# Performance work log

Hardware: AMD Instinct MI355X
Metric: run time of the kernel (lower is better)

## Reference

```python
import jax, jax.numpy as jnp
import numpy as np

OUT_SIZE = 7          # output_size
RATIO = 2             # sampling_ratio
STRIDES = (4, 8, 16, 32)  # feature_map_strides, levels P2..P5
CANONICAL = 224.0


def _bilinear_sample(fm, ys, xs):
    """fm: [H,W,C]; ys: [R,K]; xs: [R,K] -> [R,K,K,C] samples at (y[r,ky], x[r,kx]).
    Out-of-range points (y<=-1 or y>=H, same for x) produce 0, matching ROIAlign."""
    H, W, C = fm.shape
    vy = (ys > -1.0) & (ys < H)
    vx = (xs > -1.0) & (xs < W)
    y = jnp.clip(ys, 0.0, H - 1.0)
    x = jnp.clip(xs, 0.0, W - 1.0)
    y0 = jnp.floor(y).astype(jnp.int32)
    x0 = jnp.floor(x).astype(jnp.int32)
    y1 = jnp.minimum(y0 + 1, H - 1)
    x1 = jnp.minimum(x0 + 1, W - 1)
    ly = y - y0; hy = 1.0 - ly  # [R,K]
    lx = x - x0; hx = 1.0 - lx
    f00 = fm[y0[:, :, None], x0[:, None, :]]  # [R,Ky,Kx,C]
    f01 = fm[y0[:, :, None], x1[:, None, :]]
    f10 = fm[y1[:, :, None], x0[:, None, :]]
    f11 = fm[y1[:, :, None], x1[:, None, :]]
    w00 = (hy[:, :, None] * hx[:, None, :])[..., None]
    w01 = (hy[:, :, None] * lx[:, None, :])[..., None]
    w10 = (ly[:, :, None] * hx[:, None, :])[..., None]
    w11 = (ly[:, :, None] * lx[:, None, :])[..., None]
    val = w00 * f00 + w01 * f01 + w10 * f10 + w11 * f11
    mask = (vy[:, :, None] & vx[:, None, :])[..., None]
    return jnp.where(mask, val, 0.0)


def _roi_align_one(fm, boxes):
    """fm: [H,W,C]; boxes: [R,4] in this feature map's coords -> [R,C,S,S]."""
    x1, y1, x2, y2 = boxes[:, 0], boxes[:, 1], boxes[:, 2], boxes[:, 3]
    rw = jnp.maximum(x2 - x1, 1.0)
    rh = jnp.maximum(y2 - y1, 1.0)
    S, r = OUT_SIZE, RATIO
    K = S * r
    g = (jnp.arange(K, dtype=jnp.float32) + 0.5) / r  # sample grid in bin units
    ys = y1[:, None] + g[None, :] * (rh / S)[:, None]  # [R,K]
    xs = x1[:, None] + g[None, :] * (rw / S)[:, None]
    v = _bilinear_sample(fm, ys, xs)                   # [R,K,K,C]
    R_ = v.shape[0]; C = fm.shape[-1]
    v = v.reshape(R_, S, r, S, r, C).mean(axis=(2, 4))  # avg over sampling points
    return v.transpose(0, 3, 1, 2)                      # [R,C,S,S]


def setup_inputs() -> dict:
    key = jax.random.key(0)
    ks = jax.random.split(key, 5)
    B, C, N = 4, 256, 512
    fm2 = jax.random.normal(ks[0], (B, 256, 256, C), dtype=jnp.float32)
    fm3 = jax.random.normal(ks[1], (B, 128, 128, C), dtype=jnp.float32)
    fm4 = jax.random.normal(ks[2], (B, 64, 64, C), dtype=jnp.float32)
    fm5 = jax.random.normal(ks[3], (B, 32, 32, C), dtype=jnp.float32)
    pts = jax.random.uniform(ks[4], (B, N, 2, 2), minval=0.0, maxval=1024.0)
    lo = jnp.min(pts, axis=2)  # [B,N,2] -> (x1,y1)
    hi = jnp.max(pts, axis=2)  # [B,N,2] -> (x2,y2)
    rois = jnp.concatenate([lo, hi], axis=-1)  # [B,N,4]
    return {"fm2": fm2, "fm3": fm3, "fm4": fm4, "fm5": fm5, "rois": rois}


def reference(fm2, fm3, fm4, fm5, rois):
    # FPN level assignment (image coords)
    x1, y1, x2, y2 = rois[..., 0], rois[..., 1], rois[..., 2], rois[..., 3]
    area = (y2 - y1) * (x2 - x1)
    lvl = jnp.log(jnp.sqrt(area) / CANONICAL) / jnp.log(2.0) + 4.0
    lvl = jnp.clip(jnp.round(lvl).astype(jnp.int32), 2, 5)  # [B,N]

    out = 0.0
    for i, (fm, stride) in enumerate(zip((fm2, fm3, fm4, fm5), STRIDES)):
        scale = 1.0 / stride
        aligned = jax.vmap(lambda f, b: _roi_align_one(f, b * scale))(fm, rois)
        out = out + jnp.where((lvl == i + 2)[:, :, None, None, None], aligned, 0.0)
    return out  # [B,N,C,S,S]
```

## Files before the change

kernel.cpp:

```cpp
#include <hip/hip_runtime.h>


constexpr int S     = 7;
constexpr int SS    = 49;
constexpr int CCH   = 256;
constexpr int NROI  = 512;
constexpr int BATCH = 4;

__global__ __launch_bounds__(512, 4) void roialign_kernel(
    const float* __restrict__ fm2, const float* __restrict__ fm3,
    const float* __restrict__ fm4, const float* __restrict__ fm5,
    const float* __restrict__ rois, float* __restrict__ out)
{
    __shared__ float    tile[SS * CCH];
    __shared__ float    s_wyh[14], s_wyl[14], s_wxh[14], s_wxl[14];
    __shared__ unsigned s_ry0[14], s_ry1[14], s_cx0[14], s_cx1[14];
    __shared__ float    s_bw[SS][4];
    __shared__ float    s_bu[SS][4];
    __shared__ unsigned s_bm[SS];

    const int roi = blockIdx.x;
    const int b   = roi >> 9;

    const float x1  = rois[roi * 4 + 0];
    const float y1v = rois[roi * 4 + 1];
    const float x2  = rois[roi * 4 + 2];
    const float y2v = rois[roi * 4 + 3];

    const float area = (y2v - y1v) * (x2 - x1);
    const float lraw = logf(sqrtf(area) * (1.0f / 224.0f)) * 1.4426950408889634f + 4.0f;
    int lvl = (int)rintf(lraw);
    lvl = lvl < 2 ? 2 : (lvl > 5 ? 5 : lvl);

    const float* fm; int H; float scale;
    if (lvl == 2)      { fm = fm2; H = 256; scale = 0.25f;    }
    else if (lvl == 3) { fm = fm3; H = 128; scale = 0.125f;   }
    else if (lvl == 4) { fm = fm4; H = 64;  scale = 0.0625f;  }
    else               { fm = fm5; H = 32;  scale = 0.03125f; }
    const int W = H;
    fm += (size_t)b * H * W * CCH;

    const float bx1 = x1 * scale, by1 = y1v * scale;
    const float rw  = fmaxf(x2 * scale - bx1, 1.0f);
    const float rh  = fmaxf(y2v * scale - by1, 1.0f);
    const float stx = rw * (1.0f / 7.0f);
    const float sty = rh * (1.0f / 7.0f);

    const int t = threadIdx.x;

    if (t < 14) {
        const int k = t;
        const float yy = by1 + ((float)k + 0.5f) * 0.5f * sty;
        const float Hf = (float)H;
        const bool  v  = (yy > -1.0f) && (yy < Hf);
        const float yc = fminf(fmaxf(yy, 0.0f), Hf - 1.0f);
        const int   y0 = (int)floorf(yc);
        const int   y1i = min(y0 + 1, H - 1);
        const float ly = yc - (float)y0;
        s_wyl[k] = v ? ly : 0.0f;
        s_wyh[k] = v ? 1.0f - ly : 0.0f;
        s_ry0[k] = (unsigned)(y0  * W * (CCH * 4));
        s_ry1[k] = (unsigned)(y1i * W * (CCH * 4));
    } else if (t >= 64 && t < 78) {
        const int k = t - 64;
        const float xx = bx1 + ((float)k + 0.5f) * 0.5f * stx;
        const float Wf = (float)W;
        const bool  v  = (xx > -1.0f) && (xx < Wf);
        const float xc = fminf(fmaxf(xx, 0.0f), Wf - 1.0f);
        const int   x0 = (int)floorf(xc);
        const int   x1i = min(x0 + 1, W - 1);
        const float lx = xc - (float)x0;
        s_wxl[k] = v ? lx : 0.0f;
        s_wxh[k] = v ? 1.0f - lx : 0.0f;
        s_cx0[k] = (unsigned)(x0  * (CCH * 4));
        s_cx1[k] = (unsigned)(x1i * (CCH * 4));
    }
    __syncthreads();

    if (t < SS) {
        const int sy = t / 7, sx = t - sy * 7;
        const int ky = sy << 1, kx = sx << 1;

        float w0 = s_wyh[ky], w1 = s_wyl[ky], w2 = s_wyh[ky + 1], w3 = s_wyl[ky + 1];
        {
            const unsigned rA = s_ry0[ky], rB = s_ry1[ky];
            const unsigned rC = s_ry0[ky + 1], rD = s_ry1[ky + 1];
            const bool eBA = (rB == rA);
            if (eBA) { w0 += w1; w1 = 0.f; }
            const bool eCA = (rC == rA);
            const bool eCB = !eCA && (rC == rB);
            if (eCA) w0 += w2; else if (eCB) w1 += w2;
            if (eCA || eCB) w2 = 0.f;
            const bool eDA = (rD == rA);
            const bool eDB = !eDA && (rD == rB);
            const bool eDC = !eDA && !eDB && (rD == rC);
            if (eDA) w0 += w3; else if (eDB) w1 += w3; else if (eDC) w2 += w3;
            if (eDA || eDB || eDC) w3 = 0.f;
        }
        float u0 = s_wxh[kx], u1 = s_wxl[kx], u2 = s_wxh[kx + 1], u3 = s_wxl[kx + 1];
        {
            const unsigned cA = s_cx0[kx], cB = s_cx1[kx];
            const unsigned cC = s_cx0[kx + 1], cD = s_cx1[kx + 1];
            const bool eBA = (cB == cA);
            if (eBA) { u0 += u1; u1 = 0.f; }
            const bool eCA = (cC == cA);
            const bool eCB = !eCA && (cC == cB);
            if (eCA) u0 += u2; else if (eCB) u1 += u2;
            if (eCA || eCB) u2 = 0.f;
            const bool eDA = (cD == cA);
            const bool eDB = !eDA && (cD == cB);
            const bool eDC = !eDA && !eDB && (cD == cC);
            if (eDA) u0 += u3; else if (eDB) u1 += u3; else if (eDC) u2 += u3;
            if (eDA || eDB || eDC) u3 = 0.f;
        }
        s_bw[t][0] = w0; s_bw[t][1] = w1; s_bw[t][2] = w2; s_bw[t][3] = w3;
        s_bu[t][0] = u0; s_bu[t][1] = u1; s_bu[t][2] = u2; s_bu[t][3] = u3;
        s_bm[t] = (w0 != 0.f ? 0x01u : 0u) | (w1 != 0.f ? 0x02u : 0u)
                | (w2 != 0.f ? 0x04u : 0u) | (w3 != 0.f ? 0x08u : 0u)
                | (u0 != 0.f ? 0x10u : 0u) | (u1 != 0.f ? 0x20u : 0u)
                | (u2 != 0.f ? 0x40u : 0u) | (u3 != 0.f ? 0x80u : 0u);
    }
    __syncthreads();

    const int lane = t & 63;
    const int wv   = t >> 6;
    const unsigned cb = (unsigned)(lane << 4);

    const char* __restrict__ fmb = (const char*)fm;
    const float4 z4 = make_float4(0.f, 0.f, 0.f, 0.f);

    for (int bin = wv; bin < SS; bin += 8) {
        const int sy = bin / 7;
        const int sx = bin - sy * 7;
        const int ky = sy << 1, kx = sx << 1;

        const unsigned m = (unsigned)__builtin_amdgcn_readfirstlane((int)s_bm[bin]);

        const float w0 = s_bw[bin][0], w1 = s_bw[bin][1];
        const float w2 = s_bw[bin][2], w3 = s_bw[bin][3];
        const float u0 = s_bu[bin][0], u1 = s_bu[bin][1];
        const float u2 = s_bu[bin][2], u3 = s_bu[bin][3];

        const unsigned rA = s_ry0[ky],     rB = s_ry1[ky];
        const unsigned rC = s_ry0[ky + 1], rD = s_ry1[ky + 1];
        const unsigned cA = s_cx0[kx],     cB = s_cx1[kx];
        const unsigned cC = s_cx0[kx + 1], cD = s_cx1[kx + 1];

#define LD4(OFF) (*(const float4*)(fmb + (OFF)))
        float4 f00 = z4, f01 = z4, f02 = z4, f03 = z4;
        float4 f10 = z4, f11 = z4, f12 = z4, f13 = z4;
        float4 f20 = z4, f21 = z4, f22 = z4, f23 = z4;
        float4 f30 = z4, f31 = z4, f32 = z4, f33 = z4;

        if ((m & 0x11u) == 0x11u) f00 = LD4(rA + cA + cb);
        if ((m & 0x21u) == 0x21u) f01 = LD4(rA + cB + cb);
        if ((m & 0x41u) == 0x41u) f02 = LD4(rA + cC + cb);
        if ((m & 0x81u) == 0x81u) f03 = LD4(rA + cD + cb);
        if ((m & 0x12u) == 0x12u) f10 = LD4(rB + cA + cb);
        if ((m & 0x22u) == 0x22u) f11 = LD4(rB + cB + cb);
        if ((m & 0x42u) == 0x42u) f12 = LD4(rB + cC + cb);
        if ((m & 0x82u) == 0x82u) f13 = LD4(rB + cD + cb);
        if ((m & 0x14u) == 0x14u) f20 = LD4(rC + cA + cb);
        if ((m & 0x24u) == 0x24u) f21 = LD4(rC + cB + cb);
        if ((m & 0x44u) == 0x44u) f22 = LD4(rC + cC + cb);
        if ((m & 0x84u) == 0x84u) f23 = LD4(rC + cD + cb);
        if ((m & 0x18u) == 0x18u) f30 = LD4(rD + cA + cb);
        if ((m & 0x28u) == 0x28u) f31 = LD4(rD + cB + cb);
        if ((m & 0x48u) == 0x48u) f32 = LD4(rD + cC + cb);
        if ((m & 0x88u) == 0x88u) f33 = LD4(rD + cD + cb);
#undef LD4
        __builtin_amdgcn_sched_barrier(0);

        float4 acc = z4;
#define ACC4(Wt, F) { const float pw_ = (Wt); \
        acc.x = fmaf(pw_, (F).x, acc.x); acc.y = fmaf(pw_, (F).y, acc.y); \
        acc.z = fmaf(pw_, (F).z, acc.z); acc.w = fmaf(pw_, (F).w, acc.w); }
        ACC4(w0 * u0, f00); ACC4(w0 * u1, f01); ACC4(w0 * u2, f02); ACC4(w0 * u3, f03);
        ACC4(w1 * u0, f10); ACC4(w1 * u1, f11); ACC4(w1 * u2, f12); ACC4(w1 * u3, f13);
        ACC4(w2 * u0, f20); ACC4(w2 * u1, f21); ACC4(w2 * u2, f22); ACC4(w2 * u3, f23);
        ACC4(w3 * u0, f30); ACC4(w3 * u1, f31); ACC4(w3 * u2, f32); ACC4(w3 * u3, f33);
#undef ACC4

        const unsigned xsw = (((unsigned)bin >> 2) & 7u) << 2;
        float* dst = &tile[bin * CCH + ((unsigned)(lane << 2) ^ xsw)];
        *(float4*)dst = make_float4(acc.x * 0.25f, acc.y * 0.25f,
                                    acc.z * 0.25f, acc.w * 0.25f);
    }

    __syncthreads();

    float* oreg = out + (size_t)roi * (CCH * SS);
    for (int i = t; i < (CCH * SS) / 4; i += 512) {
        const int f0 = i * 4;
        float4 v;
        {
            const int f = f0 + 0;
            const int c = f / SS, bn = f - c * SS;
            v.x = tile[bn * CCH + (c ^ ((((unsigned)bn >> 2) & 7u) << 2))];
        }
        {
            const int f = f0 + 1;
            const int c = f / SS, bn = f - c * SS;
            v.y = tile[bn * CCH + (c ^ ((((unsigned)bn >> 2) & 7u) << 2))];
        }
        {
            const int f = f0 + 2;
            const int c = f / SS, bn = f - c * SS;
            v.z = tile[bn * CCH + (c ^ ((((unsigned)bn >> 2) & 7u) << 2))];
        }
        {
            const int f = f0 + 3;
            const int c = f / SS, bn = f - c * SS;
            v.w = tile[bn * CCH + (c ^ ((((unsigned)bn >> 2) & 7u) << 2))];
        }
        *(float4*)(oreg + f0) = v;
    }
}

extern "C" void kernel_launch(void* const* d_in, const int* in_sizes, int n_in,
                              void* d_out, int out_size, void* d_ws, size_t ws_size,
                              hipStream_t stream) {
    const float* fm2  = (const float*)d_in[0];
    const float* fm3  = (const float*)d_in[1];
    const float* fm4  = (const float*)d_in[2];
    const float* fm5  = (const float*)d_in[3];
    const float* rois = (const float*)d_in[4];
    float* out = (float*)d_out;

    roialign_kernel<<<BATCH * NROI, 512, 0, stream>>>(fm2, fm3, fm4, fm5, rois, out);
}
```

Measured before the change: 64.26 us.

## Split channel processing into two halves to halve LDS tile and raise occupancy

Processes the 256 channels in two passes of 128, using float2 loads per lane and a half-size LDS tile, so more blocks fit per CU (launch bounds raised to 8). Per-bin weights and offsets are forced into scalar registers via readfirstlane. In exchange, each block runs two gather/transpose passes with extra barriers and narrower 8-byte global loads, which may reduce per-load efficiency.

```diff
diff --git a/kernel.cpp b/kernel.cpp
--- a/kernel.cpp
+++ b/kernel.cpp
@@ -4,15 +4,23 @@
 constexpr int S     = 7;
 constexpr int SS    = 49;
 constexpr int CCH   = 256;
+constexpr int HCH   = 128;
 constexpr int NROI  = 512;
 constexpr int BATCH = 4;
 
-__global__ __launch_bounds__(512, 4) void roialign_kernel(
+__device__ __forceinline__ float rflf(float x) {
+    return __int_as_float(__builtin_amdgcn_readfirstlane(__float_as_int(x)));
+}
+__device__ __forceinline__ unsigned rflu(unsigned x) {
+    return (unsigned)__builtin_amdgcn_readfirstlane((int)x);
+}
+
+__global__ __launch_bounds__(512, 8) void roialign_kernel(
     const float* __restrict__ fm2, const float* __restrict__ fm3,
     const float* __restrict__ fm4, const float* __restrict__ fm5,
     const float* __restrict__ rois, float* __restrict__ out)
 {
-    __shared__ float    tile[SS * CCH];
+    __shared__ float    tile[SS * HCH];
     __shared__ float    s_wyh[14], s_wyl[14], s_wxh[14], s_wxl[14];
     __shared__ unsigned s_ry0[14], s_ry1[14], s_cx0[14], s_cx1[14];
     __shared__ float    s_bw[SS][4];
@@ -124,96 +132,96 @@
 
     const int lane = t & 63;
     const int wv   = t >> 6;
-    const unsigned cb = (unsigned)(lane << 4);
-
     const char* __restrict__ fmb = (const char*)fm;
-    const float4 z4 = make_float4(0.f, 0.f, 0.f, 0.f);
-
-    for (int bin = wv; bin < SS; bin += 8) {
-        const int sy = bin / 7;
-        const int sx = bin - sy * 7;
-        const int ky = sy << 1, kx = sx << 1;
-
-        const unsigned m = (unsigned)__builtin_amdgcn_readfirstlane((int)s_bm[bin]);
-
-        const float w0 = s_bw[bin][0], w1 = s_bw[bin][1];
-        const float w2 = s_bw[bin][2], w3 = s_bw[bin][3];
-        const float u0 = s_bu[bin][0], u1 = s_bu[bin][1];
-        const float u2 = s_bu[bin][2], u3 = s_bu[bin][3];
-
-        const unsigned rA = s_ry0[ky],     rB = s_ry1[ky];
-        const unsigned rC = s_ry0[ky + 1], rD = s_ry1[ky + 1];
-        const unsigned cA = s_cx0[kx],     cB = s_cx1[kx];
-        const unsigned cC = s_cx0[kx + 1], cD = s_cx1[kx + 1];
-
-#define LD4(OFF) (*(const float4*)(fmb + (OFF)))
-        float4 f00 = z4, f01 = z4, f02 = z4, f03 = z4;
-        float4 f10 = z4, f11 = z4, f12 = z4, f13 = z4;
-        float4 f20 = z4, f21 = z4, f22 = z4, f23 = z4;
-        float4 f30 = z4, f31 = z4, f32 = z4, f33 = z4;
-
-        if ((m & 0x11u) == 0x11u) f00 = LD4(rA + cA + cb);
-        if ((m & 0x21u) == 0x21u) f01 = LD4(rA + cB + cb);
-        if ((m & 0x41u) == 0x41u) f02 = LD4(rA + cC + cb);
-        if ((m & 0x81u) == 0x81u) f03 = LD4(rA + cD + cb);
-        if ((m & 0x12u) == 0x12u) f10 = LD4(rB + cA + cb);
-        if ((m & 0x22u) == 0x22u) f11 = LD4(rB + cB + cb);
-        if ((m & 0x42u) == 0x42u) f12 = LD4(rB + cC + cb);
-        if ((m & 0x82u) == 0x82u) f13 = LD4(rB + cD + cb);
-        if ((m & 0x14u) == 0x14u) f20 = LD4(rC + cA + cb);
-        if ((m & 0x24u) == 0x24u) f21 = LD4(rC + cB + cb);
-        if ((m & 0x44u) == 0x44u) f22 = LD4(rC + cC + cb);
-        if ((m & 0x84u) == 0x84u) f23 = LD4(rC + cD + cb);
-        if ((m & 0x18u) == 0x18u) f30 = LD4(rD + cA + cb);
-        if ((m & 0x28u) == 0x28u) f31 = LD4(rD + cB + cb);
-        if ((m & 0x48u) == 0x48u) f32 = LD4(rD + cC + cb);
-        if ((m & 0x88u) == 0x88u) f33 = LD4(rD + cD + cb);
-#undef LD4
-        __builtin_amdgcn_sched_barrier(0);
-
-        float4 acc = z4;
-#define ACC4(Wt, F) { const float pw_ = (Wt); \
-        acc.x = fmaf(pw_, (F).x, acc.x); acc.y = fmaf(pw_, (F).y, acc.y); \
-        acc.z = fmaf(pw_, (F).z, acc.z); acc.w = fmaf(pw_, (F).w, acc.w); }
-        ACC4(w0 * u0, f00); ACC4(w0 * u1, f01); ACC4(w0 * u2, f02); ACC4(w0 * u3, f03);
-        ACC4(w1 * u0, f10); ACC4(w1 * u1, f11); ACC4(w1 * u2, f12); ACC4(w1 * u3, f13);
-        ACC4(w2 * u0, f20); ACC4(w2 * u1, f21); ACC4(w2 * u2, f22); ACC4(w2 * u3, f23);
-        ACC4(w3 * u0, f30); ACC4(w3 * u1, f31); ACC4(w3 * u2, f32); ACC4(w3 * u3, f33);
-#undef ACC4
-
-        const unsigned xsw = (((unsigned)bin >> 2) & 7u) << 2;
-        float* dst = &tile[bin * CCH + ((unsigned)(lane << 2) ^ xsw)];
-        *(float4*)dst = make_float4(acc.x * 0.25f, acc.y * 0.25f,
-                                    acc.z * 0.25f, acc.w * 0.25f);
-    }
-
-    __syncthreads();
-
-    float* oreg = out + (size_t)roi * (CCH * SS);
-    for (int i = t; i < (CCH * SS) / 4; i += 512) {
-        const int f0 = i * 4;
-        float4 v;
-        {
-            const int f = f0 + 0;
-            const int c = f / SS, bn = f - c * SS;
-            v.x = tile[bn * CCH + (c ^ ((((unsigned)bn >> 2) & 7u) << 2))];
-        }
-        {
-            const int f = f0 + 1;
-            const int c = f / SS, bn = f - c * SS;
-            v.y = tile[bn * CCH + (c ^ ((((unsigned)bn >> 2) & 7u) << 2))];
-        }
-        {
-            const int f = f0 + 2;
-            const int c = f / SS, bn = f - c * SS;
-            v.z = tile[bn * CCH + (c ^ ((((unsigned)bn >> 2) & 7u) << 2))];
-        }
-        {
-            const int f = f0 + 3;
-            const int c = f / SS, bn = f - c * SS;
-            v.w = tile[bn * CCH + (c ^ ((((unsigned)bn >> 2) & 7u) << 2))];
-        }
-        *(float4*)(oreg + f0) = v;
+    const float2 z2 = make_float2(0.f, 0.f);
+
+    for (int half = 0; half < 2; ++half) {
+        const unsigned cb = (unsigned)((half << 9) + (lane << 3));
+
+        for (int bin = wv; bin < SS; bin += 8) {
+            const int sy = bin / 7;
+            const int sx = bin - sy * 7;
+            const int ky = sy << 1, kx = sx << 1;
+
+            const unsigned m  = rflu(s_bm[bin]);
+            const float w0 = rflf(s_bw[bin][0]), w1 = rflf(s_bw[bin][1]);
+            const float w2 = rflf(s_bw[bin][2]), w3 = rflf(s_bw[bin][3]);
+            const float u0 = rflf(s_bu[bin][0]), u1 = rflf(s_bu[bin][1]);
+            const float u2 = rflf(s_bu[bin][2]), u3 = rflf(s_bu[bin][3]);
+            const unsigned rA = rflu(s_ry0[ky]),     rB = rflu(s_ry1[ky]);
+            const unsigned rC = rflu(s_ry0[ky + 1]), rD = rflu(s_ry1[ky + 1]);
+            const unsigned cA = rflu(s_cx0[kx]),     cB = rflu(s_cx1[kx]);
+            const unsigned cC = rflu(s_cx0[kx + 1]), cD = rflu(s_cx1[kx + 1]);
+
+#define LD2(OFF) (*(const float2*)(fmb + (OFF)))
+            float2 f00 = z2, f01 = z2, f02 = z2, f03 = z2;
+            float2 f10 = z2, f11 = z2, f12 = z2, f13 = z2;
+            float2 f20 = z2, f21 = z2, f22 = z2, f23 = z2;
+            float2 f30 = z2, f31 = z2, f32 = z2, f33 = z2;
+
+            if ((m & 0x11u) == 0x11u) f00 = LD2(rA + cA + cb);
+            if ((m & 0x21u) == 0x21u) f01 = LD2(rA + cB + cb);
+            if ((m & 0x41u) == 0x41u) f02 = LD2(rA + cC + cb);
+            if ((m & 0x81u) == 0x81u) f03 = LD2(rA + cD + cb);
+            if ((m & 0x12u) == 0x12u) f10 = LD2(rB + cA + cb);
+            if ((m & 0x22u) == 0x22u) f11 = LD2(rB + cB + cb);
+            if ((m & 0x42u) == 0x42u) f12 = LD2(rB + cC + cb);
+            if ((m & 0x82u) == 0x82u) f13 = LD2(rB + cD + cb);
+            if ((m & 0x14u) == 0x14u) f20 = LD2(rC + cA + cb);
+            if ((m & 0x24u) == 0x24u) f21 = LD2(rC + cB + cb);
+            if ((m & 0x44u) == 0x44u) f22 = LD2(rC + cC + cb);
+            if ((m & 0x84u) == 0x84u) f23 = LD2(rC + cD + cb);
+            if ((m & 0x18u) == 0x18u) f30 = LD2(rD + cA + cb);
+            if ((m & 0x28u) == 0x28u) f31 = LD2(rD + cB + cb);
+            if ((m & 0x48u) == 0x48u) f32 = LD2(rD + cC + cb);
+            if ((m & 0x88u) == 0x88u) f33 = LD2(rD + cD + cb);
+#undef LD2
+            __builtin_amdgcn_sched_barrier(0);
+
+            float2 acc = z2;
+#define ACC2(Wt, F) { const float pw_ = (Wt); \
+            acc.x = fmaf(pw_, (F).x, acc.x); acc.y = fmaf(pw_, (F).y, acc.y); }
+            ACC2(w0 * u0, f00); ACC2(w0 * u1, f01); ACC2(w0 * u2, f02); ACC2(w0 * u3, f03);
+            ACC2(w1 * u0, f10); ACC2(w1 * u1, f11); ACC2(w1 * u2, f12); ACC2(w1 * u3, f13);
+            ACC2(w2 * u0, f20); ACC2(w2 * u1, f21); ACC2(w2 * u2, f22); ACC2(w2 * u3, f23);
+            ACC2(w3 * u0, f30); ACC2(w3 * u1, f31); ACC2(w3 * u2, f32); ACC2(w3 * u3, f33);
+#undef ACC2
+
+            const unsigned csw = ((unsigned)(lane << 1)) ^ (((unsigned)bin & 15u) << 1);
+            *(float2*)&tile[bin * HCH + csw] =
+                make_float2(acc.x * 0.25f, acc.y * 0.25f);
+        }
+
+        __syncthreads();
+
+        float* oreg = out + (size_t)roi * (CCH * SS) + (size_t)half * (HCH * SS);
+        for (int i = t; i < (HCH * SS) / 4; i += 512) {
+            const int f0 = i * 4;
+            float4 v;
+            {
+                const int f = f0 + 0;
+                const int c = f / SS, bn = f - c * SS;
+                v.x = tile[bn * HCH + (c ^ (((unsigned)bn & 15u) << 1))];
+            }
+            {
+                const int f = f0 + 1;
+                const int c = f / SS, bn = f - c * SS;
+                v.y = tile[bn * HCH + (c ^ (((unsigned)bn & 15u) << 1))];
+            }
+            {
+                const int f = f0 + 2;
+                const int c = f / SS, bn = f - c * SS;
+                v.z = tile[bn * HCH + (c ^ (((unsigned)bn & 15u) << 1))];
+            }
+            {
+                const int f = f0 + 3;
+                const int c = f / SS, bn = f - c * SS;
+                v.w = tile[bn * HCH + (c ^ (((unsigned)bn & 15u) << 1))];
+            }
+            *(float4*)(oreg + f0) = v;
+        }
+
+        __syncthreads();
     }
 }
 
```

Result: slower. 78.66 us (+22.4%).

## Separate row/column bilinear weights and reuse horizontally interpolated rows across bins

Applied to the files above, without the earlier changes.

Splits the bilinear weights into per-row and per-column sets and assigns one wave per output column (7 waves, 448 threads). Each wave walks the 7 bin rows and keeps a two-entry cache of horizontally interpolated feature rows. This lets it skip reloading a feature row already fetched for the previous bin row, which cuts global loads and FMAs. The cost is fewer waves per block, a serial loop over rows with more live registers, and dropping the min-blocks launch bound hint.

```diff
diff --git a/kernel.cpp b/kernel.cpp
--- a/kernel.cpp
+++ b/kernel.cpp
@@ -7,7 +7,11 @@
 constexpr int NROI  = 512;
 constexpr int BATCH = 4;
 
-__global__ __launch_bounds__(512, 4) void roialign_kernel(
+__device__ __forceinline__ unsigned rflu(unsigned x) {
+    return (unsigned)__builtin_amdgcn_readfirstlane((int)x);
+}
+
+__global__ __launch_bounds__(448) void roialign_kernel(
     const float* __restrict__ fm2, const float* __restrict__ fm3,
     const float* __restrict__ fm4, const float* __restrict__ fm5,
     const float* __restrict__ rois, float* __restrict__ out)
@@ -15,9 +19,12 @@
     __shared__ float    tile[SS * CCH];
     __shared__ float    s_wyh[14], s_wyl[14], s_wxh[14], s_wxl[14];
     __shared__ unsigned s_ry0[14], s_ry1[14], s_cx0[14], s_cx1[14];
-    __shared__ float    s_bw[SS][4];
-    __shared__ float    s_bu[SS][4];
-    __shared__ unsigned s_bm[SS];
+    __shared__ float    s_rw[7][4];
+    __shared__ unsigned s_rr[7][4];
+    __shared__ unsigned s_rm[7];
+    __shared__ float    s_cw[7][4];
+    __shared__ unsigned s_cc[7][4];
+    __shared__ unsigned s_cm[7];
 
     const int roi = blockIdx.x;
     const int b   = roi >> 9;
@@ -77,14 +84,12 @@
     }
     __syncthreads();
 
-    if (t < SS) {
-        const int sy = t / 7, sx = t - sy * 7;
-        const int ky = sy << 1, kx = sx << 1;
-
+    if (t < 7) {
+        const int ky = t << 1;
         float w0 = s_wyh[ky], w1 = s_wyl[ky], w2 = s_wyh[ky + 1], w3 = s_wyl[ky + 1];
-        {
-            const unsigned rA = s_ry0[ky], rB = s_ry1[ky];
-            const unsigned rC = s_ry0[ky + 1], rD = s_ry1[ky + 1];
+        const unsigned rA = s_ry0[ky], rB = s_ry1[ky];
+        const unsigned rC = s_ry0[ky + 1], rD = s_ry1[ky + 1];
+        {
             const bool eBA = (rB == rA);
             if (eBA) { w0 += w1; w1 = 0.f; }
             const bool eCA = (rC == rA);
@@ -97,10 +102,17 @@
             if (eDA) w0 += w3; else if (eDB) w1 += w3; else if (eDC) w2 += w3;
             if (eDA || eDB || eDC) w3 = 0.f;
         }
+        s_rw[t][0] = w0; s_rw[t][1] = w1; s_rw[t][2] = w2; s_rw[t][3] = w3;
+        s_rr[t][0] = rA; s_rr[t][1] = rB; s_rr[t][2] = rC; s_rr[t][3] = rD;
+        s_rm[t] = (w0 != 0.f ? 1u : 0u) | (w1 != 0.f ? 2u : 0u)
+                | (w2 != 0.f ? 4u : 0u) | (w3 != 0.f ? 8u : 0u);
+    } else if (t >= 64 && t < 71) {
+        const int sx = t - 64;
+        const int kx = sx << 1;
         float u0 = s_wxh[kx], u1 = s_wxl[kx], u2 = s_wxh[kx + 1], u3 = s_wxl[kx + 1];
-        {
-            const unsigned cA = s_cx0[kx], cB = s_cx1[kx];
-            const unsigned cC = s_cx0[kx + 1], cD = s_cx1[kx + 1];
+        const unsigned cA = s_cx0[kx], cB = s_cx1[kx];
+        const unsigned cC = s_cx0[kx + 1], cD = s_cx1[kx + 1];
+        {
             const bool eBA = (cB == cA);
             if (eBA) { u0 += u1; u1 = 0.f; }
             const bool eCA = (cC == cA);
@@ -113,107 +125,136 @@
             if (eDA) u0 += u3; else if (eDB) u1 += u3; else if (eDC) u2 += u3;
             if (eDA || eDB || eDC) u3 = 0.f;
         }
-        s_bw[t][0] = w0; s_bw[t][1] = w1; s_bw[t][2] = w2; s_bw[t][3] = w3;
-        s_bu[t][0] = u0; s_bu[t][1] = u1; s_bu[t][2] = u2; s_bu[t][3] = u3;
-        s_bm[t] = (w0 != 0.f ? 0x01u : 0u) | (w1 != 0.f ? 0x02u : 0u)
-                | (w2 != 0.f ? 0x04u : 0u) | (w3 != 0.f ? 0x08u : 0u)
-                | (u0 != 0.f ? 0x10u : 0u) | (u1 != 0.f ? 0x20u : 0u)
-                | (u2 != 0.f ? 0x40u : 0u) | (u3 != 0.f ? 0x80u : 0u);
+        s_cw[sx][0] = u0; s_cw[sx][1] = u1; s_cw[sx][2] = u2; s_cw[sx][3] = u3;
+        s_cc[sx][0] = cA; s_cc[sx][1] = cB; s_cc[sx][2] = cC; s_cc[sx][3] = cD;
+        s_cm[sx] = (u0 != 0.f ? 1u : 0u) | (u1 != 0.f ? 2u : 0u)
+                 | (u2 != 0.f ? 4u : 0u) | (u3 != 0.f ? 8u : 0u);
     }
     __syncthreads();
 
     const int lane = t & 63;
     const int wv   = t >> 6;
     const unsigned cb = (unsigned)(lane << 4);
-
     const char* __restrict__ fmb = (const char*)fm;
     const float4 z4 = make_float4(0.f, 0.f, 0.f, 0.f);
 
-    for (int bin = wv; bin < SS; bin += 8) {
-        const int sy = bin / 7;
-        const int sx = bin - sy * 7;
-        const int ky = sy << 1, kx = sx << 1;
-
-        const unsigned m = (unsigned)__builtin_amdgcn_readfirstlane((int)s_bm[bin]);
-
-        const float w0 = s_bw[bin][0], w1 = s_bw[bin][1];
-        const float w2 = s_bw[bin][2], w3 = s_bw[bin][3];
-        const float u0 = s_bu[bin][0], u1 = s_bu[bin][1];
-        const float u2 = s_bu[bin][2], u3 = s_bu[bin][3];
-
-        const unsigned rA = s_ry0[ky],     rB = s_ry1[ky];
-        const unsigned rC = s_ry0[ky + 1], rD = s_ry1[ky + 1];
-        const unsigned cA = s_cx0[kx],     cB = s_cx1[kx];
-        const unsigned cC = s_cx0[kx + 1], cD = s_cx1[kx + 1];
+    const unsigned cmask = rflu(s_cm[wv]);
+    const unsigned c0 = rflu(s_cc[wv][0]), c1 = rflu(s_cc[wv][1]);
+    const unsigned c2 = rflu(s_cc[wv][2]), c3 = rflu(s_cc[wv][3]);
+    const float u0 = s_cw[wv][0], u1 = s_cw[wv][1];
+    const float u2 = s_cw[wv][2], u3 = s_cw[wv][3];
+
+    unsigned idA = 0xFFFFFFFFu, idB = 0xFFFFFFFFu;
+    float4 xrA = z4, xrB = z4;
+
+    float4 p00 = z4, p01 = z4, p02 = z4, p03 = z4;
+    float4 p10 = z4, p11 = z4, p12 = z4, p13 = z4;
+    float4 p20 = z4, p21 = z4, p22 = z4, p23 = z4;
+    float4 p30 = z4, p31 = z4, p32 = z4, p33 = z4;
 
 #define LD4(OFF) (*(const float4*)(fmb + (OFF)))
-        float4 f00 = z4, f01 = z4, f02 = z4, f03 = z4;
-        float4 f10 = z4, f11 = z4, f12 = z4, f13 = z4;
-        float4 f20 = z4, f21 = z4, f22 = z4, f23 = z4;
-        float4 f30 = z4, f31 = z4, f32 = z4, f33 = z4;
-
-        if ((m & 0x11u) == 0x11u) f00 = LD4(rA + cA + cb);
-        if ((m & 0x21u) == 0x21u) f01 = LD4(rA + cB + cb);
-        if ((m & 0x41u) == 0x41u) f02 = LD4(rA + cC + cb);
-        if ((m & 0x81u) == 0x81u) f03 = LD4(rA + cD + cb);
-        if ((m & 0x12u) == 0x12u) f10 = LD4(rB + cA + cb);
-        if ((m & 0x22u) == 0x22u) f11 = LD4(rB + cB + cb);
-        if ((m & 0x42u) == 0x42u) f12 = LD4(rB + cC + cb);
-        if ((m & 0x82u) == 0x82u) f13 = LD4(rB + cD + cb);
-        if ((m & 0x14u) == 0x14u) f20 = LD4(rC + cA + cb);
-        if ((m & 0x24u) == 0x24u) f21 = LD4(rC + cB + cb);
-        if ((m & 0x44u) == 0x44u) f22 = LD4(rC + cC + cb);
-        if ((m & 0x84u) == 0x84u) f23 = LD4(rC + cD + cb);
-        if ((m & 0x18u) == 0x18u) f30 = LD4(rD + cA + cb);
-        if ((m & 0x28u) == 0x28u) f31 = LD4(rD + cB + cb);
-        if ((m & 0x48u) == 0x48u) f32 = LD4(rD + cC + cb);
-        if ((m & 0x88u) == 0x88u) f33 = LD4(rD + cD + cb);
-#undef LD4
+#define XR4(DST, P0, P1, P2, P3) \
+    DST.x = fmaf(u0,(P0).x, fmaf(u1,(P1).x, fmaf(u2,(P2).x, u3*(P3).x))); \
+    DST.y = fmaf(u0,(P0).y, fmaf(u1,(P1).y, fmaf(u2,(P2).y, u3*(P3).y))); \
+    DST.z = fmaf(u0,(P0).z, fmaf(u1,(P1).z, fmaf(u2,(P2).z, u3*(P3).z))); \
+    DST.w = fmaf(u0,(P0).w, fmaf(u1,(P1).w, fmaf(u2,(P2).w, u3*(P3).w)));
+
+    #pragma unroll
+    for (int sy = 0; sy < 7; ++sy) {
+        const unsigned rmask = rflu(s_rm[sy]);
+        const unsigned r0 = rflu(s_rr[sy][0]), r1 = rflu(s_rr[sy][1]);
+        const unsigned r2 = rflu(s_rr[sy][2]), r3 = rflu(s_rr[sy][3]);
+        const float w0 = s_rw[sy][0], w1 = s_rw[sy][1];
+        const float w2 = s_rw[sy][2], w3 = s_rw[sy][3];
+
+        const bool h0A = (r0 == idA), h0B = (r0 == idB);
+        const bool h1A = (r1 == idA), h1B = (r1 == idB);
+        const bool h2A = (r2 == idA), h2B = (r2 == idB);
+        const bool h3A = (r3 == idA), h3B = (r3 == idB);
+        const bool f0 = (rmask & 1u) && !h0A && !h0B;
+        const bool f1 = (rmask & 2u) && !h1A && !h1B;
+        const bool f2 = (rmask & 4u) && !h2A && !h2B;
+        const bool f3 = (rmask & 8u) && !h3A && !h3B;
+
+        if (f0) {
+            if (cmask & 1u) p00 = LD4(r0 + c0 + cb);
+            if (cmask & 2u) p01 = LD4(r0 + c1 + cb);
+            if (cmask & 4u) p02 = LD4(r0 + c2 + cb);
+            if (cmask & 8u) p03 = LD4(r0 + c3 + cb);
+        }
+        if (f1) {
+            if (cmask & 1u) p10 = LD4(r1 + c0 + cb);
+            if (cmask & 2u) p11 = LD4(r1 + c1 + cb);
+            if (cmask & 4u) p12 = LD4(r1 + c2 + cb);
+            if (cmask & 8u) p13 = LD4(r1 + c3 + cb);
+        }
+        if (f2) {
+            if (cmask & 1u) p20 = LD4(r2 + c0 + cb);
+            if (cmask & 2u) p21 = LD4(r2 + c1 + cb);
+            if (cmask & 4u) p22 = LD4(r2 + c2 + cb);
+            if (cmask & 8u) p23 = LD4(r2 + c3 + cb);
+        }
+        if (f3) {
+            if (cmask & 1u) p30 = LD4(r3 + c0 + cb);
+            if (cmask & 2u) p31 = LD4(r3 + c1 + cb);
+            if (cmask & 4u) p32 = LD4(r3 + c2 + cb);
+            if (cmask & 8u) p33 = LD4(r3 + c3 + cb);
+        }
         __builtin_amdgcn_sched_barrier(0);
 
-        float4 acc = z4;
-#define ACC4(Wt, F) { const float pw_ = (Wt); \
-        acc.x = fmaf(pw_, (F).x, acc.x); acc.y = fmaf(pw_, (F).y, acc.y); \
-        acc.z = fmaf(pw_, (F).z, acc.z); acc.w = fmaf(pw_, (F).w, acc.w); }
-        ACC4(w0 * u0, f00); ACC4(w0 * u1, f01); ACC4(w0 * u2, f02); ACC4(w0 * u3, f03);
-        ACC4(w1 * u0, f10); ACC4(w1 * u1, f11); ACC4(w1 * u2, f12); ACC4(w1 * u3, f13);
-        ACC4(w2 * u0, f20); ACC4(w2 * u1, f21); ACC4(w2 * u2, f22); ACC4(w2 * u3, f23);
-        ACC4(w3 * u0, f30); ACC4(w3 * u1, f31); ACC4(w3 * u2, f32); ACC4(w3 * u3, f33);
-#undef ACC4
-
+        float4 xr0, xr1, xr2, xr3;
+        if (h0A) xr0 = xrA; else if (h0B) xr0 = xrB; else { XR4(xr0, p00, p01, p02, p03); }
+        if (h1A) xr1 = xrA; else if (h1B) xr1 = xrB; else { XR4(xr1, p10, p11, p12, p13); }
+        if (h2A) xr2 = xrA; else if (h2B) xr2 = xrB; else { XR4(xr2, p20, p21, p22, p23); }
+        if (h3A) xr3 = xrA; else if (h3B) xr3 = xrB; else { XR4(xr3, p30, p31, p32, p33); }
+
+        float4 acc;
+        acc.x = fmaf(w0, xr0.x, fmaf(w1, xr1.x, fmaf(w2, xr2.x, w3 * xr3.x)));
+        acc.y = fmaf(w0, xr0.y, fmaf(w1, xr1.y, fmaf(w2, xr2.y, w3 * xr3.y)));
+        acc.z = fmaf(w0, xr0.z, fmaf(w1, xr1.z, fmaf(w2, xr2.z, w3 * xr3.z)));
+        acc.w = fmaf(w0, xr0.w, fmaf(w1, xr1.w, fmaf(w2, xr2.w, w3 * xr3.w)));
+
+        const int bin = sy * 7 + wv;
         const unsigned xsw = (((unsigned)bin >> 2) & 7u) << 2;
         float* dst = &tile[bin * CCH + ((unsigned)(lane << 2) ^ xsw)];
         *(float4*)dst = make_float4(acc.x * 0.25f, acc.y * 0.25f,
                                     acc.z * 0.25f, acc.w * 0.25f);
-    }
+
+        if (rmask & 1u) { idB = idA; xrB = xrA; idA = r0; xrA = xr0; }
+        if (rmask & 2u) { idB = idA; xrB = xrA; idA = r1; xrA = xr1; }
+        if (rmask & 4u) { idB = idA; xrB = xrA; idA = r2; xrA = xr2; }
+        if (rmask & 8u) { idB = idA; xrB = xrA; idA = r3; xrA = xr3; }
+    }
+#undef LD4
+#undef XR4
 
     __syncthreads();
 
     float* oreg = out + (size_t)roi * (CCH * SS);
-    for (int i = t; i < (CCH * SS) / 4; i += 512) {
-        const int f0 = i * 4;
+    for (int i = t; i < (CCH * SS) / 4; i += 448) {
+        const int f0i = i * 4;
         float4 v;
         {
-            const int f = f0 + 0;
+            const int f = f0i + 0;
             const int c = f / SS, bn = f - c * SS;
             v.x = tile[bn * CCH + (c ^ ((((unsigned)bn >> 2) & 7u) << 2))];
         }
         {
-            const int f = f0 + 1;
+            const int f = f0i + 1;
             const int c = f / SS, bn = f - c * SS;
             v.y = tile[bn * CCH + (c ^ ((((unsigned)bn >> 2) & 7u) << 2))];
         }
         {
-            const int f = f0 + 2;
+            const int f = f0i + 2;
             const int c = f / SS, bn = f - c * SS;
             v.z = tile[bn * CCH + (c ^ ((((unsigned)bn >> 2) & 7u) << 2))];
         }
         {
-            const int f = f0 + 3;
+            const int f = f0i + 3;
             const int c = f / SS, bn = f - c * SS;
             v.w = tile[bn * CCH + (c ^ ((((unsigned)bn >> 2) & 7u) << 2))];
         }
-        *(float4*)(oreg + f0) = v;
+        *(float4*)(oreg + f0i) = v;
     }
 }
 
@@ -227,5 +268,5 @@
     const float* rois = (const float*)d_in[4];
     float* out = (float*)d_out;
 
-    roialign_kernel<<<BATCH * NROI, 512, 0, stream>>>(fm2, fm3, fm4, fm5, rois, out);
+    roialign_kernel<<<BATCH * NROI, 448, 0, stream>>>(fm2, fm3, fm4, fm5, rois, out);
 }
```

Measured after the change: 101.1 us. 57.3% more time.
